# Optimization experiments

Measured on AMD Instinct MI355X. Metric: run time of the kernel, lower is better.

Reference implementation:

```python
import jax, jax.numpy as jnp
import numpy as np

B, T, C, K, V = 4, 2048, 1024, 1024, 1024
SQRT_K = float(np.sqrt(K))


def setup_inputs() -> dict:
    key = jax.random.key(0)
    ks = jax.random.split(key, 7)
    s = 0.02
    return {
        "x": jax.random.normal(ks[0], (B, T, C), jnp.float32),
        "Wq": (jax.random.normal(ks[1], (C, K), jnp.float32) * s),
        "bq": jnp.zeros((K,), jnp.float32),
        "Wk": (jax.random.normal(ks[2], (C, K), jnp.float32) * s),
        "bk": jnp.zeros((K,), jnp.float32),
        "Wv": (jax.random.normal(ks[3], (C, V), jnp.float32) * s),
        "bv": jnp.zeros((V,), jnp.float32),
    }


def reference(x, Wq, bq, Wk, bk, Wv, bv):
    # projections: [B,T,C] @ [C,K] -> [B,T,K]
    q = x @ Wq + bq
    k = x @ Wk + bk
    v = x @ Wv + bv
    # logits[b,t,s] = q[b,t,:] . k[b,s,:]
    logits = jnp.einsum("btk,bsk->bts", q, k)
    # original mask: mask[j,i] = 1 if i > j -> strict upper triangle masked to -inf
    seq = logits.shape[1]
    mask = jnp.triu(jnp.ones((seq, seq), bool), k=1)
    logits = jnp.where(mask[None, :, :], -jnp.inf, logits)
    # NOTE: original softmax is over dim=1 (query axis), not the key axis
    probs = jax.nn.softmax(logits / SQRT_K, axis=1)
    read = jnp.einsum("bts,bsv->btv", probs, v)
    return jnp.concatenate((x, read), axis=2)
```

## Files before the change

kernel.cpp:

```cpp
#include <hip/hip_runtime.h>
#include <hip/hip_bf16.h>
#include <stdint.h>

#define DEVI __device__ __forceinline__

using u16 = unsigned short;
typedef __attribute__((ext_vector_type(8))) _Float16 halfx8;
typedef __attribute__((ext_vector_type(4))) float f32x4;

constexpr int BB = 4, TT = 2048, CC = 1024, KD = 1024, VD = 1024;
constexpr int QKVW = 3072;
constexpr int OUTW = CC + VD;
constexpr float INV_SQRT_K = 0.03125f;

DEVI u16 f2h(float f) {
  _Float16 h = (_Float16)f;
  return __builtin_bit_cast(u16, h);
}
DEVI float h2f(u16 u) {
  return (float)__builtin_bit_cast(_Float16, u);
}

DEVI void gload16(const u16* g, u16* l) {
  __builtin_amdgcn_global_load_lds(
      (const __attribute__((address_space(1))) void*)g,
      (__attribute__((address_space(3))) void*)l, 16, 0, 0);
}

__global__ void cast_x_copy(const float* __restrict__ x, u16* __restrict__ xh,
                            float* __restrict__ out) {
  size_t i = (size_t)blockIdx.x * blockDim.x + threadIdx.x;
  float4 v = reinterpret_cast<const float4*>(x)[i];
  ushort4 u;
  u.x = f2h(v.x); u.y = f2h(v.y); u.z = f2h(v.z); u.w = f2h(v.w);
  reinterpret_cast<ushort4*>(xh)[i] = u;
  size_t e = i * 4;
  size_t bt = e / CC;
  int c = (int)(e % CC);
  *reinterpret_cast<float4*>(&out[bt * OUTW + c]) = v;
}

__global__ void transpose_cast_w(const float* __restrict__ W, u16* __restrict__ Wt) {
  __shared__ float tile[32][33];
  int n0 = blockIdx.x * 32, c0 = blockIdx.y * 32;
  int tx = threadIdx.x, ty = threadIdx.y;
  for (int i = ty; i < 32; i += 8)
    tile[i][tx] = W[(size_t)(c0 + i) * KD + n0 + tx];
  __syncthreads();
  for (int i = ty; i < 32; i += 8)
    Wt[(size_t)(n0 + i) * CC + c0 + tx] = f2h(tile[tx][i]);
}

__global__ void concat_bias(const float* __restrict__ bq, const float* __restrict__ bk,
                            const float* __restrict__ bv, float* __restrict__ bc) {
  int n = blockIdx.x * 256 + threadIdx.x;
  float v = (n < 1024) ? bq[n] : (n < 2048) ? bk[n - 1024] : bv[n - 2048];
  bc[n] = v;
}

__global__ void transpose_v(const u16* __restrict__ QKV, u16* __restrict__ Vt) {
  __shared__ u16 tile[32][33];
  int b = blockIdx.z;
  int n0 = blockIdx.x * 32, s0 = blockIdx.y * 32;
  const u16* src = QKV + (size_t)b * TT * QKVW + 2048;
  u16* dst = Vt + (size_t)b * VD * TT;
  int tx = threadIdx.x, ty = threadIdx.y;
  for (int i = ty; i < 32; i += 8)
    tile[i][tx] = src[(size_t)(s0 + i) * QKVW + n0 + tx];
  __syncthreads();
  for (int i = ty; i < 32; i += 8)
    dst[(size_t)(n0 + i) * TT + s0 + tx] = tile[tx][i];
}

template <typename OutT, int BN, int SWZ, bool CSKIP, bool KLIM, bool BIAS, bool FSTAT>
__global__ __launch_bounds__(512, 2) void gemm_bt(
    const u16* __restrict__ A, const u16* __restrict__ Bm, OutT* __restrict__ Out,
    const float* __restrict__ bias, float* __restrict__ Mp, float* __restrict__ Dp,
    int Kd, int lda, int ldb, int ldo,
    long long strA, long long strB, long long strO, float alpha) {
  constexpr int BM = 256, BK = 32;
  constexpr int WM = (BN == 256) ? 2 : 4, WN = 8 / WM;
  constexpr int WR = BM / WM, WC = BN / WN;
  constexpr int MR = WR / 16, NR = WC / 16;
  constexpr int BLINES = BN / 128;
  constexpr int LPT = 2 + BLINES;
  constexpr int ASZ = BM * BK, BSZ = BN * BK;
  __shared__ u16 sA[3 * ASZ];
  __shared__ u16 sB[3 * BSZ];
  __shared__ float redm[2][256];
  __shared__ float reds[2][256];

  int bx = blockIdx.x, by = blockIdx.y;
  if constexpr (SWZ == 1) {
    const int gx = gridDim.x;
    const int nx = gx >> 3;
    int fid = bx + gx * by;
    int xcd = fid & 7, idx = fid >> 3;
    bx = xcd * nx + idx % nx;
    by = idx / nx;
  }
  const int r0 = bx * BM, c0 = by * BN;
  if (CSKIP && c0 > r0 + BM - 1) return;
  A   += (size_t)blockIdx.z * strA;
  Bm  += (size_t)blockIdx.z * strB;
  Out += (size_t)blockIdx.z * strO;

  const int tid = threadIdx.x;
  const int lane = tid & 63;
  const int w = tid >> 6;
  const int wm = w / WN, wn = w % WN;
  const int l15 = lane & 15, l4 = lane >> 4;
  const int cswz8 = 8 * (l4 ^ ((l15 >> 1) & 3));

  const int srow = tid >> 2;
  const int sc8 = 8 * ((tid & 3) ^ ((tid >> 3) & 3));
  const u16* gA  = A  + (size_t)(r0 + srow) * lda + sc8;
  const u16* gA2 = gA + (size_t)128 * lda;
  const u16* gB  = Bm + (size_t)(c0 + srow) * ldb + sc8;
  const u16* gB2 = gB + (size_t)128 * ldb;
  const int sdst = tid * 8;

  f32x4 acc[MR][NR] = {};

  int kmax = Kd;
  if (KLIM) { int km = r0 + BM; kmax = km < Kd ? km : Kd; }
  const int NT = kmax / BK;

  auto stage = [&](int buf, int kt) {
    const int k0 = kt * BK;
    u16* da = sA + buf * ASZ + sdst;
    gload16(gA + k0, da);
    gload16(gA2 + k0, da + 4096);
    u16* db = sB + buf * BSZ + sdst;
    gload16(gB + k0, db);
    if (BLINES == 2) gload16(gB2 + k0, db + 4096);
  };

  stage(0, 0);
  stage(1, 1);
  if constexpr (LPT == 4) asm volatile("s_waitcnt vmcnt(4)" ::: "memory");
  else                    asm volatile("s_waitcnt vmcnt(3)" ::: "memory");
  __builtin_amdgcn_s_barrier();

  int buf = 0;
  for (int kt = 0; kt < NT; ++kt) {
    int nb = buf + 2; if (nb >= 3) nb -= 3;
    const u16* rA = sA + buf * ASZ;
    const u16* rB = sB + buf * BSZ;
    halfx8 af[MR], bfv[NR];
#pragma unroll
    for (int n = 0; n < NR; ++n)
      bfv[n] = *reinterpret_cast<const halfx8*>(&rB[(wn * WC + n * 16 + l15) * BK + cswz8]);
#pragma unroll
    for (int m = 0; m < MR; ++m)
      af[m] = *reinterpret_cast<const halfx8*>(&rA[(wm * WR + m * 16 + l15) * BK + cswz8]);
    if (kt + 2 < NT) stage(nb, kt + 2);
    __builtin_amdgcn_s_setprio(1);
#pragma unroll
    for (int m = 0; m < MR; ++m)
#pragma unroll
      for (int n = 0; n < NR; ++n)
        acc[m][n] = __builtin_amdgcn_mfma_f32_16x16x32_f16(af[m], bfv[n], acc[m][n], 0, 0, 0);
    __builtin_amdgcn_s_setprio(0);
    if (kt + 2 < NT) {
      if constexpr (LPT == 4) asm volatile("s_waitcnt vmcnt(4)" ::: "memory");
      else                    asm volatile("s_waitcnt vmcnt(3)" ::: "memory");
    } else if (kt + 1 < NT) {
      asm volatile("s_waitcnt vmcnt(0)" ::: "memory");
    }
    if (kt + 1 < NT) __builtin_amdgcn_s_barrier();
    buf = buf + 1; if (buf == 3) buf = 0;
  }

#pragma unroll
  for (int m = 0; m < MR; ++m) {
    const int growb = r0 + wm * WR + m * 16 + l4 * 4;
#pragma unroll
    for (int n = 0; n < NR; ++n) {
      const int gcol = c0 + wn * WC + n * 16 + l15;
      float bvv = 0.f;
      if (BIAS) bvv = bias[gcol];
#pragma unroll
      for (int r = 0; r < 4; ++r) {
        float val = acc[m][n][r] * alpha + bvv;
        size_t off = (size_t)(growb + r) * ldo + gcol;
        if constexpr (sizeof(OutT) == 2) {
          reinterpret_cast<u16*>(Out)[off] = f2h(val);
        } else {
          reinterpret_cast<float*>(Out)[off] = val;
        }
      }
    }
  }

  if constexpr (FSTAT) {
#pragma unroll
    for (int n = 0; n < NR; ++n) {
      const int gcol = c0 + wn * WC + n * 16 + l15;
      float mx = -1e30f;
#pragma unroll
      for (int m = 0; m < MR; ++m) {
        const int growb = r0 + wm * WR + m * 16 + l4 * 4;
#pragma unroll
        for (int r = 0; r < 4; ++r)
          if (growb + r >= gcol) mx = fmaxf(mx, acc[m][n][r] * alpha);
      }
      mx = fmaxf(mx, __shfl_xor(mx, 16));
      mx = fmaxf(mx, __shfl_xor(mx, 32));
      float sm = 0.f;
#pragma unroll
      for (int m = 0; m < MR; ++m) {
        const int growb = r0 + wm * WR + m * 16 + l4 * 4;
#pragma unroll
        for (int r = 0; r < 4; ++r)
          if (growb + r >= gcol) sm += __expf(acc[m][n][r] * alpha - mx);
      }
      sm += __shfl_xor(sm, 16);
      sm += __shfl_xor(sm, 32);
      if (l4 == 0) {
        redm[wm][wn * WC + n * 16 + l15] = mx;
        reds[wm][wn * WC + n * 16 + l15] = sm;
      }
    }
    __syncthreads();
    if (tid < BN) {
      float m0 = redm[0][tid], m1 = redm[1][tid];
      float m2 = fmaxf(m0, m1);
      float d2 = reds[0][tid] * __expf(m0 - m2) + reds[1][tid] * __expf(m1 - m2);
      const int rt = r0 >> 8;
      Mp[((size_t)rt * BB + blockIdx.z) * TT + c0 + tid] = m2;
      Dp[((size_t)rt * BB + blockIdx.z) * TT + c0 + tid] = d2;
    }
  }
}

__global__ void stats_combine(const float* __restrict__ Mp, const float* __restrict__ Dp,
                              float* __restrict__ Mc, float* __restrict__ Di) {
  int b = blockIdx.y;
  int s = blockIdx.x * 256 + threadIdx.x;
  int rt0 = s >> 8;
  float m = -1e30f;
  for (int rt = rt0; rt < TT / 256; ++rt)
    m = fmaxf(m, Mp[((size_t)rt * BB + b) * TT + s]);
  float d = 0.f;
  for (int rt = rt0; rt < TT / 256; ++rt)
    d += Dp[((size_t)rt * BB + b) * TT + s] * __expf(Mp[((size_t)rt * BB + b) * TT + s] - m);
  Mc[b * TT + s] = m;
  Di[b * TT + s] = 1.f / d;
}

constexpr int ATCH = 64;
__global__ void softmax_apply(u16* __restrict__ SP, const float* __restrict__ Mc,
                              const float* __restrict__ Di) {
  int b = blockIdx.z;
  int s = blockIdx.x * 256 + threadIdx.x;
  int s0 = blockIdx.x * 256;
  int t0 = blockIdx.y * ATCH;
  if (s0 > ((t0 + ATCH - 1) | 255)) return;
  u16* Sb = SP + (size_t)b * TT * TT;
  float m = Mc[b * TT + s], di = Di[b * TT + s];
  for (int t = t0; t < t0 + ATCH; ++t) {
    float p = 0.f;
    if (t >= s) p = __expf(h2f(Sb[(size_t)t * TT + s]) - m) * di;
    Sb[(size_t)t * TT + s] = f2h(p);
  }
}

extern "C" void kernel_launch(void* const* d_in, const int* in_sizes, int n_in,
                              void* d_out, int out_size, void* d_ws, size_t ws_size,
                              hipStream_t stream) {
  const float* x  = (const float*)d_in[0];
  const float* Wq = (const float*)d_in[1];
  const float* bq = (const float*)d_in[2];
  const float* Wk = (const float*)d_in[3];
  const float* bk = (const float*)d_in[4];
  const float* Wv = (const float*)d_in[5];
  const float* bv = (const float*)d_in[6];
  float* out = (float*)d_out;
  char* ws = (char*)d_ws;
  constexpr size_t MB = 1024ull * 1024ull;

  u16* xh   = (u16*)(ws);
  u16* QKV  = (u16*)(ws + 16 * MB);
  u16* Wt   = (u16*)(ws + 64 * MB);
  float* bc = (float*)(ws + 70 * MB);
  u16* SP   = (u16*)(ws + 71 * MB);
  u16* Vt = xh;
  float* Mp = (float*)(ws + 64 * MB);
  float* Dp = (float*)(ws + 65 * MB);
  float* Mc = (float*)(ws + 66 * MB);
  float* Di = (float*)(ws + 66 * MB + 64 * 1024);

  cast_x_copy<<<dim3((BB * TT * CC / 4) / 256), dim3(256), 0, stream>>>(x, xh, out);
  dim3 tb(32, 8);
  transpose_cast_w<<<dim3(KD / 32, CC / 32), tb, 0, stream>>>(Wq, Wt);
  transpose_cast_w<<<dim3(KD / 32, CC / 32), tb, 0, stream>>>(Wk, Wt + 1024 * 1024);
  transpose_cast_w<<<dim3(VD / 32, CC / 32), tb, 0, stream>>>(Wv, Wt + 2048 * 1024);
  concat_bias<<<dim3(QKVW / 256), 256, 0, stream>>>(bq, bk, bv, bc);

  gemm_bt<u16, 256, 1, false, false, true, false><<<dim3(32, QKVW / 256, 1), 512, 0, stream>>>(
      xh, Wt, QKV, bc, nullptr, nullptr, CC, CC, CC, QKVW, 0, 0, 0, 1.f);

  transpose_v<<<dim3(VD / 32, TT / 32, BB), tb, 0, stream>>>(QKV, Vt);

  gemm_bt<u16, 256, 0, true, false, false, true><<<dim3(TT / 256, TT / 256, BB), 512, 0, stream>>>(
      QKV, QKV + 1024, SP, nullptr, Mp, Dp, KD, QKVW, QKVW, TT,
      (long long)TT * QKVW, (long long)TT * QKVW, (long long)TT * TT, INV_SQRT_K);

  stats_combine<<<dim3(TT / 256, BB), 256, 0, stream>>>(Mp, Dp, Mc, Di);
  softmax_apply<<<dim3(TT / 256, TT / ATCH, BB), 256, 0, stream>>>(SP, Mc, Di);

  gemm_bt<float, 128, 0, false, true, false, false><<<dim3(TT / 256, VD / 128, BB), 512, 0, stream>>>(
      SP, Vt, out + CC, nullptr, nullptr, nullptr, TT, TT, TT, OUTW,
      (long long)TT * TT, (long long)VD * TT, (long long)TT * OUTW, 1.f);
}
```

Baseline: 218.2 us.

## Drop max-subtraction, write exp scores directly, fold normalization into V scaling

After: 194.1 us. -11.0%, faster.

```diff
diff --git a/kernel.cpp b/kernel.cpp
--- a/kernel.cpp
+++ b/kernel.cpp
@@ -6,6 +6,7 @@
 
 using u16 = unsigned short;
 typedef __attribute__((ext_vector_type(8))) _Float16 halfx8;
+typedef __attribute__((ext_vector_type(8))) unsigned short u16x8;
 typedef __attribute__((ext_vector_type(4))) float f32x4;
 
 constexpr int BB = 4, TT = 2048, CC = 1024, KD = 1024, VD = 1024;
@@ -72,23 +73,20 @@
     dst[(size_t)(n0 + i) * TT + s0 + tx] = tile[tx][i];
 }
 
-template <typename OutT, int BN, int SWZ, bool CSKIP, bool KLIM, bool BIAS, bool FSTAT>
+template <typename OutT, int SWZ, bool CSKIP, bool KLIM, bool BIAS, bool CMASK>
 __global__ __launch_bounds__(512, 2) void gemm_bt(
     const u16* __restrict__ A, const u16* __restrict__ Bm, OutT* __restrict__ Out,
-    const float* __restrict__ bias, float* __restrict__ Mp, float* __restrict__ Dp,
+    const float* __restrict__ bias, float* __restrict__ Dp,
     int Kd, int lda, int ldb, int ldo,
     long long strA, long long strB, long long strO, float alpha) {
-  constexpr int BM = 256, BK = 32;
-  constexpr int WM = (BN == 256) ? 2 : 4, WN = 8 / WM;
-  constexpr int WR = BM / WM, WC = BN / WN;
-  constexpr int MR = WR / 16, NR = WC / 16;
-  constexpr int BLINES = BN / 128;
-  constexpr int LPT = 2 + BLINES;
+  constexpr int BM = 256, BN = 128, BK = 32;
+  constexpr int WM = 4, WN = 2;
+  constexpr int WR = 64, WC = 64;
+  constexpr int MR = 4, NR = 4;
   constexpr int ASZ = BM * BK, BSZ = BN * BK;
   __shared__ u16 sA[3 * ASZ];
   __shared__ u16 sB[3 * BSZ];
-  __shared__ float redm[2][256];
-  __shared__ float reds[2][256];
+  __shared__ float reds[CMASK ? WM : 1][CMASK ? BN : 1];
 
   int bx = blockIdx.x, by = blockIdx.y;
   if constexpr (SWZ == 1) {
@@ -117,7 +115,6 @@
   const u16* gA  = A  + (size_t)(r0 + srow) * lda + sc8;
   const u16* gA2 = gA + (size_t)128 * lda;
   const u16* gB  = Bm + (size_t)(c0 + srow) * ldb + sc8;
-  const u16* gB2 = gB + (size_t)128 * ldb;
   const int sdst = tid * 8;
 
   f32x4 acc[MR][NR] = {};
@@ -133,13 +130,11 @@
     gload16(gA2 + k0, da + 4096);
     u16* db = sB + buf * BSZ + sdst;
     gload16(gB + k0, db);
-    if (BLINES == 2) gload16(gB2 + k0, db + 4096);
   };
 
   stage(0, 0);
   stage(1, 1);
-  if constexpr (LPT == 4) asm volatile("s_waitcnt vmcnt(4)" ::: "memory");
-  else                    asm volatile("s_waitcnt vmcnt(3)" ::: "memory");
+  asm volatile("s_waitcnt vmcnt(3)" ::: "memory");
   __builtin_amdgcn_s_barrier();
 
   int buf = 0;
@@ -162,108 +157,82 @@
       for (int n = 0; n < NR; ++n)
         acc[m][n] = __builtin_amdgcn_mfma_f32_16x16x32_f16(af[m], bfv[n], acc[m][n], 0, 0, 0);
     __builtin_amdgcn_s_setprio(0);
-    if (kt + 2 < NT) {
-      if constexpr (LPT == 4) asm volatile("s_waitcnt vmcnt(4)" ::: "memory");
-      else                    asm volatile("s_waitcnt vmcnt(3)" ::: "memory");
-    } else if (kt + 1 < NT) {
-      asm volatile("s_waitcnt vmcnt(0)" ::: "memory");
-    }
+    if (kt + 2 < NT)      asm volatile("s_waitcnt vmcnt(3)" ::: "memory");
+    else if (kt + 1 < NT) asm volatile("s_waitcnt vmcnt(0)" ::: "memory");
     if (kt + 1 < NT) __builtin_amdgcn_s_barrier();
     buf = buf + 1; if (buf == 3) buf = 0;
   }
 
-#pragma unroll
-  for (int m = 0; m < MR; ++m) {
-    const int growb = r0 + wm * WR + m * 16 + l4 * 4;
+  if constexpr (CMASK) {
 #pragma unroll
     for (int n = 0; n < NR; ++n) {
       const int gcol = c0 + wn * WC + n * 16 + l15;
-      float bvv = 0.f;
-      if (BIAS) bvv = bias[gcol];
-#pragma unroll
-      for (int r = 0; r < 4; ++r) {
-        float val = acc[m][n][r] * alpha + bvv;
-        size_t off = (size_t)(growb + r) * ldo + gcol;
-        if constexpr (sizeof(OutT) == 2) {
-          reinterpret_cast<u16*>(Out)[off] = f2h(val);
-        } else {
-          reinterpret_cast<float*>(Out)[off] = val;
+      float sm = 0.f;
+#pragma unroll
+      for (int m = 0; m < MR; ++m) {
+        const int growb = r0 + wm * WR + m * 16 + l4 * 4;
+#pragma unroll
+        for (int r = 0; r < 4; ++r) {
+          float p = 0.f;
+          if (growb + r >= gcol) p = __expf(acc[m][n][r] * alpha);
+          reinterpret_cast<u16*>(Out)[(size_t)(growb + r) * ldo + gcol] = f2h(p);
+          sm += p;
+        }
+      }
+      sm += __shfl_xor(sm, 16);
+      sm += __shfl_xor(sm, 32);
+      if (l4 == 0) reds[wm][wn * WC + n * 16 + l15] = sm;
+    }
+    __syncthreads();
+    if (tid < BN) {
+      float d2 = 0.f;
+#pragma unroll
+      for (int i = 0; i < WM; ++i) d2 += reds[i][tid];
+      Dp[((size_t)(r0 >> 8) * BB + blockIdx.z) * TT + c0 + tid] = d2;
+    }
+  } else {
+#pragma unroll
+    for (int m = 0; m < MR; ++m) {
+      const int growb = r0 + wm * WR + m * 16 + l4 * 4;
+#pragma unroll
+      for (int n = 0; n < NR; ++n) {
+        const int gcol = c0 + wn * WC + n * 16 + l15;
+        float bvv = 0.f;
+        if (BIAS) bvv = bias[gcol];
+#pragma unroll
+        for (int r = 0; r < 4; ++r) {
+          float val = acc[m][n][r] * alpha + bvv;
+          size_t off = (size_t)(growb + r) * ldo + gcol;
+          if constexpr (sizeof(OutT) == 2) {
+            reinterpret_cast<u16*>(Out)[off] = f2h(val);
+          } else {
+            reinterpret_cast<float*>(Out)[off] = val;
+          }
         }
       }
     }
   }
-
-  if constexpr (FSTAT) {
-#pragma unroll
-    for (int n = 0; n < NR; ++n) {
-      const int gcol = c0 + wn * WC + n * 16 + l15;
-      float mx = -1e30f;
-#pragma unroll
-      for (int m = 0; m < MR; ++m) {
-        const int growb = r0 + wm * WR + m * 16 + l4 * 4;
-#pragma unroll
-        for (int r = 0; r < 4; ++r)
-          if (growb + r >= gcol) mx = fmaxf(mx, acc[m][n][r] * alpha);
-      }
-      mx = fmaxf(mx, __shfl_xor(mx, 16));
-      mx = fmaxf(mx, __shfl_xor(mx, 32));
-      float sm = 0.f;
-#pragma unroll
-      for (int m = 0; m < MR; ++m) {
-        const int growb = r0 + wm * WR + m * 16 + l4 * 4;
-#pragma unroll
-        for (int r = 0; r < 4; ++r)
-          if (growb + r >= gcol) sm += __expf(acc[m][n][r] * alpha - mx);
-      }
-      sm += __shfl_xor(sm, 16);
-      sm += __shfl_xor(sm, 32);
-      if (l4 == 0) {
-        redm[wm][wn * WC + n * 16 + l15] = mx;
-        reds[wm][wn * WC + n * 16 + l15] = sm;
-      }
-    }
-    __syncthreads();
-    if (tid < BN) {
-      float m0 = redm[0][tid], m1 = redm[1][tid];
-      float m2 = fmaxf(m0, m1);
-      float d2 = reds[0][tid] * __expf(m0 - m2) + reds[1][tid] * __expf(m1 - m2);
-      const int rt = r0 >> 8;
-      Mp[((size_t)rt * BB + blockIdx.z) * TT + c0 + tid] = m2;
-      Dp[((size_t)rt * BB + blockIdx.z) * TT + c0 + tid] = d2;
-    }
-  }
-}
-
-__global__ void stats_combine(const float* __restrict__ Mp, const float* __restrict__ Dp,
-                              float* __restrict__ Mc, float* __restrict__ Di) {
+}
+
+__global__ void stats_combine(const float* __restrict__ Dp, float* __restrict__ Di) {
   int b = blockIdx.y;
   int s = blockIdx.x * 256 + threadIdx.x;
   int rt0 = s >> 8;
-  float m = -1e30f;
-  for (int rt = rt0; rt < TT / 256; ++rt)
-    m = fmaxf(m, Mp[((size_t)rt * BB + b) * TT + s]);
   float d = 0.f;
   for (int rt = rt0; rt < TT / 256; ++rt)
-    d += Dp[((size_t)rt * BB + b) * TT + s] * __expf(Mp[((size_t)rt * BB + b) * TT + s] - m);
-  Mc[b * TT + s] = m;
+    d += Dp[((size_t)rt * BB + b) * TT + s];
   Di[b * TT + s] = 1.f / d;
 }
 
-constexpr int ATCH = 64;
-__global__ void softmax_apply(u16* __restrict__ SP, const float* __restrict__ Mc,
-                              const float* __restrict__ Di) {
-  int b = blockIdx.z;
-  int s = blockIdx.x * 256 + threadIdx.x;
-  int s0 = blockIdx.x * 256;
-  int t0 = blockIdx.y * ATCH;
-  if (s0 > ((t0 + ATCH - 1) | 255)) return;
-  u16* Sb = SP + (size_t)b * TT * TT;
-  float m = Mc[b * TT + s], di = Di[b * TT + s];
-  for (int t = t0; t < t0 + ATCH; ++t) {
-    float p = 0.f;
-    if (t >= s) p = __expf(h2f(Sb[(size_t)t * TT + s]) - m) * di;
-    Sb[(size_t)t * TT + s] = f2h(p);
-  }
+__global__ void scale_vt(u16* __restrict__ Vt, const float* __restrict__ Di) {
+  size_t i = ((size_t)blockIdx.x * 256 + threadIdx.x) * 8;
+  int b = (int)(i >> 21);
+  int s = (int)(i & (TT - 1));
+  u16x8 v = *reinterpret_cast<u16x8*>(&Vt[i]);
+  const float* Db = Di + b * TT + s;
+#pragma unroll
+  for (int j = 0; j < 8; ++j) v[j] = f2h(h2f(v[j]) * Db[j]);
+  *reinterpret_cast<u16x8*>(&Vt[i]) = v;
 }
 
 extern "C" void kernel_launch(void* const* d_in, const int* in_sizes, int n_in,
@@ -286,10 +255,8 @@
   float* bc = (float*)(ws + 70 * MB);
   u16* SP   = (u16*)(ws + 71 * MB);
   u16* Vt = xh;
-  float* Mp = (float*)(ws + 64 * MB);
-  float* Dp = (float*)(ws + 65 * MB);
-  float* Mc = (float*)(ws + 66 * MB);
-  float* Di = (float*)(ws + 66 * MB + 64 * 1024);
+  float* Dp = (float*)(ws + 64 * MB);
+  float* Di = (float*)(ws + 65 * MB);
 
   cast_x_copy<<<dim3((BB * TT * CC / 4) / 256), dim3(256), 0, stream>>>(x, xh, out);
   dim3 tb(32, 8);
@@ -298,19 +265,19 @@
   transpose_cast_w<<<dim3(VD / 32, CC / 32), tb, 0, stream>>>(Wv, Wt + 2048 * 1024);
   concat_bias<<<dim3(QKVW / 256), 256, 0, stream>>>(bq, bk, bv, bc);
 
-  gemm_bt<u16, 256, 1, false, false, true, false><<<dim3(32, QKVW / 256, 1), 512, 0, stream>>>(
-      xh, Wt, QKV, bc, nullptr, nullptr, CC, CC, CC, QKVW, 0, 0, 0, 1.f);
+  gemm_bt<u16, 1, false, false, true, false><<<dim3(32, QKVW / 128, 1), 512, 0, stream>>>(
+      xh, Wt, QKV, bc, nullptr, CC, CC, CC, QKVW, 0, 0, 0, 1.f);
 
   transpose_v<<<dim3(VD / 32, TT / 32, BB), tb, 0, stream>>>(QKV, Vt);
 
-  gemm_bt<u16, 256, 0, true, false, false, true><<<dim3(TT / 256, TT / 256, BB), 512, 0, stream>>>(
-      QKV, QKV + 1024, SP, nullptr, Mp, Dp, KD, QKVW, QKVW, TT,
+  gemm_bt<u16, 0, true, false, false, true><<<dim3(TT / 256, TT / 128, BB), 512, 0, stream>>>(
+      QKV, QKV + 1024, SP, nullptr, Dp, KD, QKVW, QKVW, TT,
       (long long)TT * QKVW, (long long)TT * QKVW, (long long)TT * TT, INV_SQRT_K);
 
-  stats_combine<<<dim3(TT / 256, BB), 256, 0, stream>>>(Mp, Dp, Mc, Di);
-  softmax_apply<<<dim3(TT / 256, TT / ATCH, BB), 256, 0, stream>>>(SP, Mc, Di);
-
-  gemm_bt<float, 128, 0, false, true, false, false><<<dim3(TT / 256, VD / 128, BB), 512, 0, stream>>>(
-      SP, Vt, out + CC, nullptr, nullptr, nullptr, TT, TT, TT, OUTW,
+  stats_combine<<<dim3(TT / 256, BB), 256, 0, stream>>>(Dp, Di);
+  scale_vt<<<dim3(BB * VD * TT / 8 / 256), 256, 0, stream>>>(Vt, Di);
+
+  gemm_bt<float, 0, false, true, false, false><<<dim3(TT / 256, VD / 128, BB), 512, 0, stream>>>(
+      SP, Vt, out + CC, nullptr, nullptr, TT, TT, TT, OUTW,
       (long long)TT * TT, (long long)VD * TT, (long long)TT * OUTW, 1.f);
 }
```
